# Kernel tuning notes

Measured on AMD Instinct MI355X. Metric: run time of the kernel, lower is better.

The kernel has to match this reference:

```python
import jax, jax.numpy as jnp
import numpy as np

FIELD_DIMS = [50000] * 24
NUM_FIELDS = len(FIELD_DIMS)
EMBED_DIM = 16
ATTN_SIZE = 32
TOTAL_VOCAB = int(np.sum(FIELD_DIMS))
OFFSETS = jnp.asarray(np.concatenate([[0], np.cumsum(FIELD_DIMS)[:-1]]), dtype=jnp.int64)
# all unordered field pairs (i < j)
_ROWS, _COLS = np.triu_indices(NUM_FIELDS, k=1)
ROWS = jnp.asarray(_ROWS)
COLS = jnp.asarray(_COLS)


def setup_inputs() -> dict:
    key = jax.random.key(0)
    ks = jax.random.split(key, 9)
    B = 16384
    x = jax.random.randint(ks[0], (B, NUM_FIELDS), 0, 50000, dtype=jnp.int64)
    s = 0.05
    return {
        "x": x,
        "embed_table": jax.random.normal(ks[1], (TOTAL_VOCAB, EMBED_DIM), jnp.float32) * s,
        "linear_table": jax.random.normal(ks[2], (TOTAL_VOCAB, 1), jnp.float32) * s,
        "linear_bias": jnp.zeros((1,), jnp.float32),
        "attn_W": jax.random.normal(ks[3], (EMBED_DIM, ATTN_SIZE), jnp.float32) * s,
        "attn_b": jnp.zeros((ATTN_SIZE,), jnp.float32),
        "proj_w": jax.random.normal(ks[4], (ATTN_SIZE, 1), jnp.float32) * s,
        "proj_b": jnp.zeros((1,), jnp.float32),
        "fc_w": jax.random.normal(ks[5], (EMBED_DIM, 1), jnp.float32) * s,
        "fc_b": jnp.zeros((1,), jnp.float32),
    }


def reference(x, embed_table, linear_table, linear_bias, attn_W, attn_b, proj_w, proj_b, fc_w, fc_b):
    idx = x + OFFSETS[None, :]                      # [B, F] global row ids
    emb = embed_table[idx]                          # [B, F, E]
    linear_term = linear_table[idx].sum(axis=1) + linear_bias  # [B, 1]
    # pairwise elementwise products
    inner = emb[:, ROWS, :] * emb[:, COLS, :]       # [B, P, E]
    # attention MLP over pairs
    h = jax.nn.relu(jnp.einsum('bpe,ea->bpa', inner, attn_W) + attn_b)  # [B, P, A]
    scores = jnp.einsum('bpa,ao->bpo', h, proj_w) + proj_b              # [B, P, 1]
    attn = jax.nn.softmax(scores, axis=1)           # softmax over pairs
    pooled = jnp.sum(attn * inner, axis=1)          # [B, E]
    cross_term = pooled @ fc_w + fc_b               # [B, 1]
    return linear_term + cross_term
```

## Files before the change

kernel.cpp:

```cpp
#include <hip/hip_runtime.h>
#include <hip/hip_bf16.h>
#include <float.h>


#define FN 24
#define ED 16
#define AS 32
#define NP 276
#define NT 9
#define LASTV 20
#define EPITCH 20
#define RPB 4
#define NTHR 256
#define FIELD_SIZE 50000

typedef __attribute__((ext_vector_type(8)))  short bf16x8;
typedef __attribute__((ext_vector_type(16))) float f32x16;
typedef __attribute__((ext_vector_type(2)))  float f32x2;

union BFR { int i[4]; bf16x8 v; };

__device__ __forceinline__ short f2bf(float x) {
    union { __hip_bfloat16 h; short s; } u;
    u.h = __float2bfloat16(x);
    return u.s;
}
__device__ __forceinline__ float waveSum64(float v) {
#pragma unroll
    for (int off = 32; off; off >>= 1) v += __shfl_xor(v, off, 64);
    return v;
}

__global__ __launch_bounds__(NTHR, 4) void afm_kernel(
    const int*   __restrict__ x,
    const float* __restrict__ embed_table,
    const float* __restrict__ linear_table,
    const float* __restrict__ linear_bias,
    const float* __restrict__ attn_W,
    const float* __restrict__ attn_b,
    const float* __restrict__ proj_w,
    const float* __restrict__ fc_w,
    const float* __restrict__ fc_b,
    float*       __restrict__ out,
    int B)
{
    __shared__ float emb_s[RPB][FN * EPITCH];
    __shared__ int   pko_s[NT * 32];

    const int tid  = threadIdx.x;
    const int wave = tid >> 6;
    const int lane = tid & 63;
    const int half = lane >> 5;
    const int col  = lane & 31;
    const int e0   = half * 8;
    const int row  = blockIdx.x * RPB + wave;
    const bool active = row < B;
    const int rowc = active ? row : (B - 1);

    for (int s = tid; s < NT * 32; s += NTHR) {
        const int p = (s < NP) ? s : (NP - 1);
        const int q = (NP - 1) - p;
        int m = (int)((sqrtf((float)(8 * q + 1)) + 1.0f) * 0.5f);
        if (m * (m + 1) / 2 <= q) ++m;
        if ((m - 1) * m / 2 > q) --m;
        const int fi = (FN - 1) - m;
        const int fj = fi + 1 + (p - (NP - m * (m + 1) / 2));
        pko_s[s] = ((fi * (EPITCH * 4)) << 16) | (fj * (EPITCH * 4));
    }

    int idxv = 0; float linv = 0.f;
    if (lane < FN) {
        idxv = x[rowc * FN + lane] + lane * FIELD_SIZE;
        linv = linear_table[idxv];
    }
    const float lin = waveSum64(linv);

    float* emb = emb_s[wave];
#pragma unroll
    for (int t = lane; t < FN * 4; t += 64) {
        const int f = t >> 2, q = t & 3;
        const int id = __shfl(idxv, f, 64);
        *(float4*)&emb[f * EPITCH + q * 4] =
            ((const float4*)(embed_table + (size_t)id * ED))[q];
    }

    bf16x8 aW;
#pragma unroll
    for (int i = 0; i < 8; ++i) aW[i] = f2bf(attn_W[(e0 + i) * AS + col]);
    f32x2 b2[8], pw2[8];
#pragma unroll
    for (int r2 = 0; r2 < 8; ++r2) {
        const int r = 2 * r2;
        const int a0 = (r & 3) + 8 * (r >> 2) + 4 * half;
        b2[r2].x  = attn_b[a0];  b2[r2].y  = attn_b[a0 + 1];
        pw2[r2].x = proj_w[a0];  pw2[r2].y = proj_w[a0 + 1];
    }
    float fcw[8];
#pragma unroll
    for (int i = 0; i < 8; ++i) fcw[i] = fc_w[e0 + i];

    __syncthreads();

    const char* embb = (const char*)emb + half * 32;
    float sc[NT], g[NT];
#pragma unroll
    for (int t = 0; t < NT; ++t) {
        const int pk = pko_s[t * 32 + col];
        const int oi = pk >> 16;
        const int oj = pk & 0xffff;
        const float4 xi0 = *(const float4*)(embb + oi);
        const float4 xi1 = *(const float4*)(embb + oi + 16);
        const float4 xj0 = *(const float4*)(embb + oj);
        const float4 xj1 = *(const float4*)(embb + oj + 16);
        const float p0 = xi0.x * xj0.x, p1 = xi0.y * xj0.y;
        const float p2 = xi0.z * xj0.z, p3 = xi0.w * xj0.w;
        const float p4 = xi1.x * xj1.x, p5 = xi1.y * xj1.y;
        const float p6 = xi1.z * xj1.z, p7 = xi1.w * xj1.w;
        float gv = p0 * fcw[0];
        gv = fmaf(p1, fcw[1], gv); gv = fmaf(p2, fcw[2], gv);
        gv = fmaf(p3, fcw[3], gv); gv = fmaf(p4, fcw[4], gv);
        gv = fmaf(p5, fcw[5], gv); gv = fmaf(p6, fcw[6], gv);
        gv = fmaf(p7, fcw[7], gv);
        g[t] = gv;
        BFR u;
        u.i[0] = __builtin_amdgcn_perm(__float_as_int(p1), __float_as_int(p0), 0x07060302);
        u.i[1] = __builtin_amdgcn_perm(__float_as_int(p3), __float_as_int(p2), 0x07060302);
        u.i[2] = __builtin_amdgcn_perm(__float_as_int(p5), __float_as_int(p4), 0x07060302);
        u.i[3] = __builtin_amdgcn_perm(__float_as_int(p7), __float_as_int(p6), 0x07060302);
        f32x16 c;
#pragma unroll
        for (int r2 = 0; r2 < 8; ++r2) { c[2 * r2] = b2[r2].x; c[2 * r2 + 1] = b2[r2].y; }
        c = __builtin_amdgcn_mfma_f32_32x32x16_bf16(aW, u.v, c, 0, 0, 0);
        f32x2 sac; sac.x = 0.f; sac.y = 0.f;
        f32x2 z2;  z2.x = 0.f;  z2.y = 0.f;
#pragma unroll
        for (int r2 = 0; r2 < 8; ++r2) {
            f32x2 h; h.x = c[2 * r2]; h.y = c[2 * r2 + 1];
            h = __builtin_elementwise_max(h, z2);
            sac = __builtin_elementwise_fma(h, pw2[r2], sac);
        }
        float s = sac.x + sac.y;
        s += __shfl_xor(s, 32, 64);
        sc[t] = s;
    }

    float mx = sc[0];
#pragma unroll
    for (int t = 1; t < NT; ++t) mx = fmaxf(mx, sc[t]);
#pragma unroll
    for (int off = 16; off; off >>= 1) mx = fmaxf(mx, __shfl_xor(mx, off, 64));
    float es[NT], ssum = 0.f;
#pragma unroll
    for (int t = 0; t < NT; ++t) {
        const bool valid = (t < NT - 1) || (col < LASTV);
        es[t] = valid ? __expf(sc[t] - mx) : 0.f;
        ssum += es[t];
    }
#pragma unroll
    for (int off = 16; off; off >>= 1) ssum += __shfl_xor(ssum, off, 64);
    const float inv = 1.f / ssum;

    float cp = 0.f;
#pragma unroll
    for (int t = 0; t < NT; ++t) cp = fmaf(es[t], g[t], cp);
    const float cross = waveSum64(cp) * inv;

    if (active && lane == 0)
        out[row] = lin + linear_bias[0] + cross + fc_b[0];
}

extern "C" void kernel_launch(void* const* d_in, const int* in_sizes, int n_in,
                              void* d_out, int out_size, void* d_ws, size_t ws_size,
                              hipStream_t stream) {
    const int*   x            = (const int*)  d_in[0];
    const float* embed_table  = (const float*)d_in[1];
    const float* linear_table = (const float*)d_in[2];
    const float* linear_bias  = (const float*)d_in[3];
    const float* attn_W       = (const float*)d_in[4];
    const float* attn_b       = (const float*)d_in[5];
    const float* proj_w       = (const float*)d_in[6];
    const float* fc_w         = (const float*)d_in[8];
    const float* fc_b         = (const float*)d_in[9];
    float* out = (float*)d_out;

    const int B = in_sizes[0] / FN;
    const int grid = (B + RPB - 1) / RPB;
    afm_kernel<<<grid, NTHR, 0, stream>>>(x, embed_table, linear_table,
                                          linear_bias, attn_W, attn_b, proj_w,
                                          fc_w, fc_b, out, B);
}
```

Baseline: 145.8 us.

## Process four rows per wave with double-buffered embedding prefetch and online softmax

Each wave now handles four batch rows and prefetches the next row's embedding and linear-table values into registers while computing the current row, writing them into a second LDS buffer. This spreads the per-block setup (pair-offset table, weights) over more rows and hides gather latency behind MFMA work. The softmax becomes an online running max/sum, which drops the score arrays but adds two exps per tile. The grid shrinks fourfold, so there are fewer waves in flight to hide latency, and register pressure goes up.

```diff
diff --git a/kernel.cpp b/kernel.cpp
--- a/kernel.cpp
+++ b/kernel.cpp
@@ -10,7 +10,7 @@
 #define NT 9
 #define LASTV 20
 #define EPITCH 20
-#define RPB 4
+#define RPW 4
 #define NTHR 256
 #define FIELD_SIZE 50000
 
@@ -25,10 +25,24 @@
     u.h = __float2bfloat16(x);
     return u.s;
 }
-__device__ __forceinline__ float waveSum64(float v) {
-#pragma unroll
-    for (int off = 32; off; off >>= 1) v += __shfl_xor(v, off, 64);
-    return v;
+
+__device__ __forceinline__ void gather_embed(const float* __restrict__ et,
+                                             int idxv, int lane,
+                                             float4& a, float4& b) {
+    const int f0 = lane >> 2, q0 = lane & 3;
+    const int id0 = __shfl(idxv, f0, 64);
+    const int id1 = __shfl(idxv, 16 + f0, 64);
+    a = ((const float4*)(et + (size_t)id0 * ED))[q0];
+    if (lane < 32)
+        b = ((const float4*)(et + (size_t)id1 * ED))[q0];
+}
+
+__device__ __forceinline__ void write_embed(float* __restrict__ buf, int lane,
+                                            const float4& a, const float4& b) {
+    const int f0 = lane >> 2, q0 = lane & 3;
+    *(float4*)&buf[f0 * EPITCH + q0 * 4] = a;
+    if (lane < 32)
+        *(float4*)&buf[(16 + f0) * EPITCH + q0 * 4] = b;
 }
 
 __global__ __launch_bounds__(NTHR, 4) void afm_kernel(
@@ -44,7 +58,7 @@
     float*       __restrict__ out,
     int B)
 {
-    __shared__ float emb_s[RPB][FN * EPITCH];
+    __shared__ float emb_s[NTHR / 64][2][FN * EPITCH];
     __shared__ int   pko_s[NT * 32];
 
     const int tid  = threadIdx.x;
@@ -53,9 +67,7 @@
     const int half = lane >> 5;
     const int col  = lane & 31;
     const int e0   = half * 8;
-    const int row  = blockIdx.x * RPB + wave;
-    const bool active = row < B;
-    const int rowc = active ? row : (B - 1);
+    const int w0   = (blockIdx.x * (NTHR / 64) + wave) * RPW;
 
     for (int s = tid; s < NT * 32; s += NTHR) {
         const int p = (s < NP) ? s : (NP - 1);
@@ -68,105 +80,119 @@
         pko_s[s] = ((fi * (EPITCH * 4)) << 16) | (fj * (EPITCH * 4));
     }
 
-    int idxv = 0; float linv = 0.f;
-    if (lane < FN) {
-        idxv = x[rowc * FN + lane] + lane * FIELD_SIZE;
-        linv = linear_table[idxv];
-    }
-    const float lin = waveSum64(linv);
-
-    float* emb = emb_s[wave];
-#pragma unroll
-    for (int t = lane; t < FN * 4; t += 64) {
-        const int f = t >> 2, q = t & 3;
-        const int id = __shfl(idxv, f, 64);
-        *(float4*)&emb[f * EPITCH + q * 4] =
-            ((const float4*)(embed_table + (size_t)id * ED))[q];
+    int idxr[RPW];
+#pragma unroll
+    for (int k = 0; k < RPW; ++k) {
+        const int r = w0 + k, rc = (r < B) ? r : (B - 1);
+        idxr[k] = (lane < FN) ? (x[rc * FN + lane] + lane * FIELD_SIZE) : 0;
     }
 
     bf16x8 aW;
 #pragma unroll
     for (int i = 0; i < 8; ++i) aW[i] = f2bf(attn_W[(e0 + i) * AS + col]);
-    f32x2 b2[8], pw2[8];
-#pragma unroll
-    for (int r2 = 0; r2 < 8; ++r2) {
-        const int r = 2 * r2;
-        const int a0 = (r & 3) + 8 * (r >> 2) + 4 * half;
-        b2[r2].x  = attn_b[a0];  b2[r2].y  = attn_b[a0 + 1];
-        pw2[r2].x = proj_w[a0];  pw2[r2].y = proj_w[a0 + 1];
+    float b16[16], pw16[16];
+#pragma unroll
+    for (int r = 0; r < 16; ++r) {
+        const int a = (r & 3) + 8 * (r >> 2) + 4 * half;
+        b16[r]  = attn_b[a];
+        pw16[r] = proj_w[a];
     }
     float fcw[8];
 #pragma unroll
     for (int i = 0; i < 8; ++i) fcw[i] = fc_w[e0 + i];
+    const float cbias = linear_bias[0] + fc_b[0];
+
+    float linv = (lane < FN) ? linear_table[idxr[0]] : 0.f;
+    {
+        float4 ga, gb;
+        gather_embed(embed_table, idxr[0], lane, ga, gb);
+        write_embed(emb_s[wave][0], lane, ga, gb);
+    }
 
     __syncthreads();
-
-    const char* embb = (const char*)emb + half * 32;
-    float sc[NT], g[NT];
-#pragma unroll
-    for (int t = 0; t < NT; ++t) {
-        const int pk = pko_s[t * 32 + col];
-        const int oi = pk >> 16;
-        const int oj = pk & 0xffff;
-        const float4 xi0 = *(const float4*)(embb + oi);
-        const float4 xi1 = *(const float4*)(embb + oi + 16);
-        const float4 xj0 = *(const float4*)(embb + oj);
-        const float4 xj1 = *(const float4*)(embb + oj + 16);
-        const float p0 = xi0.x * xj0.x, p1 = xi0.y * xj0.y;
-        const float p2 = xi0.z * xj0.z, p3 = xi0.w * xj0.w;
-        const float p4 = xi1.x * xj1.x, p5 = xi1.y * xj1.y;
-        const float p6 = xi1.z * xj1.z, p7 = xi1.w * xj1.w;
-        float gv = p0 * fcw[0];
-        gv = fmaf(p1, fcw[1], gv); gv = fmaf(p2, fcw[2], gv);
-        gv = fmaf(p3, fcw[3], gv); gv = fmaf(p4, fcw[4], gv);
-        gv = fmaf(p5, fcw[5], gv); gv = fmaf(p6, fcw[6], gv);
-        gv = fmaf(p7, fcw[7], gv);
-        g[t] = gv;
-        BFR u;
-        u.i[0] = __builtin_amdgcn_perm(__float_as_int(p1), __float_as_int(p0), 0x07060302);
-        u.i[1] = __builtin_amdgcn_perm(__float_as_int(p3), __float_as_int(p2), 0x07060302);
-        u.i[2] = __builtin_amdgcn_perm(__float_as_int(p5), __float_as_int(p4), 0x07060302);
-        u.i[3] = __builtin_amdgcn_perm(__float_as_int(p7), __float_as_int(p6), 0x07060302);
-        f32x16 c;
-#pragma unroll
-        for (int r2 = 0; r2 < 8; ++r2) { c[2 * r2] = b2[r2].x; c[2 * r2 + 1] = b2[r2].y; }
-        c = __builtin_amdgcn_mfma_f32_32x32x16_bf16(aW, u.v, c, 0, 0, 0);
-        f32x2 sac; sac.x = 0.f; sac.y = 0.f;
-        f32x2 z2;  z2.x = 0.f;  z2.y = 0.f;
-#pragma unroll
-        for (int r2 = 0; r2 < 8; ++r2) {
-            f32x2 h; h.x = c[2 * r2]; h.y = c[2 * r2 + 1];
-            h = __builtin_elementwise_max(h, z2);
-            sac = __builtin_elementwise_fma(h, pw2[r2], sac);
+    int pk[NT];
+#pragma unroll
+    for (int t = 0; t < NT; ++t) pk[t] = pko_s[t * 32 + col];
+
+#pragma unroll
+    for (int k = 0; k < RPW; ++k) {
+        const int row = w0 + k;
+        float4 na, nb; float linn = 0.f;
+        if (k + 1 < RPW) {
+            linn = (lane < FN) ? linear_table[idxr[k + 1]] : 0.f;
+            gather_embed(embed_table, idxr[k + 1], lane, na, nb);
         }
-        float s = sac.x + sac.y;
-        s += __shfl_xor(s, 32, 64);
-        sc[t] = s;
-    }
-
-    float mx = sc[0];
-#pragma unroll
-    for (int t = 1; t < NT; ++t) mx = fmaxf(mx, sc[t]);
-#pragma unroll
-    for (int off = 16; off; off >>= 1) mx = fmaxf(mx, __shfl_xor(mx, off, 64));
-    float es[NT], ssum = 0.f;
-#pragma unroll
-    for (int t = 0; t < NT; ++t) {
-        const bool valid = (t < NT - 1) || (col < LASTV);
-        es[t] = valid ? __expf(sc[t] - mx) : 0.f;
-        ssum += es[t];
-    }
-#pragma unroll
-    for (int off = 16; off; off >>= 1) ssum += __shfl_xor(ssum, off, 64);
-    const float inv = 1.f / ssum;
-
-    float cp = 0.f;
-#pragma unroll
-    for (int t = 0; t < NT; ++t) cp = fmaf(es[t], g[t], cp);
-    const float cross = waveSum64(cp) * inv;
-
-    if (active && lane == 0)
-        out[row] = lin + linear_bias[0] + cross + fc_b[0];
+
+        const char* embb = (const char*)emb_s[wave][k & 1] + half * 32;
+        float m = -FLT_MAX, ssum = 0.f, gacc = 0.f;
+#pragma unroll
+        for (int t = 0; t < NT; ++t) {
+            const int oi = pk[t] >> 16;
+            const int oj = pk[t] & 0xffff;
+            const float4 xi0 = *(const float4*)(embb + oi);
+            const float4 xi1 = *(const float4*)(embb + oi + 16);
+            const float4 xj0 = *(const float4*)(embb + oj);
+            const float4 xj1 = *(const float4*)(embb + oj + 16);
+            const float p0 = xi0.x * xj0.x, p1 = xi0.y * xj0.y;
+            const float p2 = xi0.z * xj0.z, p3 = xi0.w * xj0.w;
+            const float p4 = xi1.x * xj1.x, p5 = xi1.y * xj1.y;
+            const float p6 = xi1.z * xj1.z, p7 = xi1.w * xj1.w;
+            float gv = p0 * fcw[0];
+            gv = fmaf(p1, fcw[1], gv); gv = fmaf(p2, fcw[2], gv);
+            gv = fmaf(p3, fcw[3], gv); gv = fmaf(p4, fcw[4], gv);
+            gv = fmaf(p5, fcw[5], gv); gv = fmaf(p6, fcw[6], gv);
+            gv = fmaf(p7, fcw[7], gv);
+            BFR u;
+            u.i[0] = __builtin_amdgcn_perm(__float_as_int(p1), __float_as_int(p0), 0x07060302);
+            u.i[1] = __builtin_amdgcn_perm(__float_as_int(p3), __float_as_int(p2), 0x07060302);
+            u.i[2] = __builtin_amdgcn_perm(__float_as_int(p5), __float_as_int(p4), 0x07060302);
+            u.i[3] = __builtin_amdgcn_perm(__float_as_int(p7), __float_as_int(p6), 0x07060302);
+            f32x16 c;
+#pragma unroll
+            for (int r = 0; r < 16; ++r) c[r] = b16[r];
+            c = __builtin_amdgcn_mfma_f32_32x32x16_bf16(aW, u.v, c, 0, 0, 0);
+            f32x2 sac; sac.x = 0.f; sac.y = 0.f;
+            f32x2 z2;  z2.x = 0.f;  z2.y = 0.f;
+#pragma unroll
+            for (int r2 = 0; r2 < 8; ++r2) {
+                f32x2 h; h.x = c[2 * r2]; h.y = c[2 * r2 + 1];
+                h = __builtin_elementwise_max(h, z2);
+                f32x2 pw; pw.x = pw16[2 * r2]; pw.y = pw16[2 * r2 + 1];
+                sac = __builtin_elementwise_fma(h, pw, sac);
+            }
+            float s = sac.x + sac.y;
+            s += __shfl_xor(s, 32, 64);
+            const bool valid = (t < NT - 1) || (col < LASTV);
+            s = valid ? s : -FLT_MAX;
+            const float mn   = fmaxf(m, s);
+            const float cold = __expf(m - mn);
+            const float e    = __expf(s - mn);
+            ssum = fmaf(ssum, cold, e);
+            gacc = fmaf(gacc, cold, e * gv);
+            m = mn;
+        }
+
+        float M = m;
+#pragma unroll
+        for (int off = 16; off; off >>= 1) M = fmaxf(M, __shfl_xor(M, off, 64));
+        const float rs = __expf(m - M);
+        ssum *= rs; gacc *= rs;
+#pragma unroll
+        for (int off = 16; off; off >>= 1) ssum += __shfl_xor(ssum, off, 64);
+#pragma unroll
+        for (int off = 32; off; off >>= 1) gacc += __shfl_xor(gacc, off, 64);
+        float lin = linv;
+#pragma unroll
+        for (int off = 32; off; off >>= 1) lin += __shfl_xor(lin, off, 64);
+
+        if (row < B && lane == 0)
+            out[row] = lin + cbias + gacc / ssum;
+
+        if (k + 1 < RPW) {
+            write_embed(emb_s[wave][(k + 1) & 1], lane, na, nb);
+            linv = linn;
+        }
+    }
 }
 
 extern "C" void kernel_launch(void* const* d_in, const int* in_sizes, int n_in,
@@ -184,7 +210,8 @@
     float* out = (float*)d_out;
 
     const int B = in_sizes[0] / FN;
-    const int grid = (B + RPB - 1) / RPB;
+    const int rows_per_block = (NTHR / 64) * RPW;
+    const int grid = (B + rows_per_block - 1) / rows_per_block;
     afm_kernel<<<grid, NTHR, 0, stream>>>(x, embed_table, linear_table,
                                           linear_bias, attn_W, attn_b, proj_w,
                                           fc_w, fc_b, out, B);
```

Measured after the change: 141.5 us. 2.9% less time.
